# Kernel tuning notes

Hardware: AMD Instinct MI355X
Metric: run time of the kernel (lower is better)

Reference implementation:

```python
import jax, jax.numpy as jnp
import numpy as np

N_TOTAL = 100000   # total nodes across types
NP_TYPE = 50000    # nodes per type
NP_G = 50000       # nodes per metapath graph
E_G = 500000       # edges per metapath graph
NH = 4             # attention heads
HD = 64            # per-head hidden dim
HID = 64           # shared hidden dim (== in_dim)
D = NH * HD        # 256, semantic attention dim
OUT = 64
T = 20000          # target nodes per metapath


def setup_inputs() -> dict:
    key = jax.random.key(0)
    ks = jax.random.split(key, 20)
    inp = {
        "features0": jax.random.normal(ks[0], (NP_TYPE, 256), jnp.float32),
        "features1": jax.random.normal(ks[1], (NP_TYPE, 256), jnp.float32),
        "fc_W": jax.random.normal(ks[2], (2, HID, 256), jnp.float32) * 0.06,
        "fc_b": jnp.zeros((2, HID), jnp.float32),
        "gat_W": jax.random.normal(ks[3], (2, 2, HID, D), jnp.float32) * 0.12,
        "attn_l": jax.random.normal(ks[4], (2, 2, NH, HD), jnp.float32) * 0.12,
        "attn_r": jax.random.normal(ks[5], (2, 2, NH, HD), jnp.float32) * 0.12,
        "sem_W": jax.random.normal(ks[6], (2, D, D), jnp.float32) * 0.06,
        "sem_b": jnp.zeros((2, D), jnp.float32),
        "sem_q": jax.random.normal(ks[7], (2, D), jnp.float32) * 0.06,
        "fcout_W": jax.random.normal(ks[8], (2, D, OUT), jnp.float32) * 0.06,
        "fcout_b": jnp.zeros((2, OUT), jnp.float32),
        # static index structure (== np.where(type_mask == i))
        "type_idx": jnp.arange(2 * NP_TYPE, dtype=jnp.int32).reshape(2, NP_TYPE),
        "node_idx": jax.random.randint(ks[9], (2, 2, NP_G), 0, N_TOTAL, jnp.int32),
        "edge_src": jax.random.randint(ks[10], (2, 2, E_G), 0, NP_G, jnp.int32),
        "edge_dst": jax.random.randint(ks[11], (2, 2, E_G), 0, NP_G, jnp.int32),
        "tgt_idx": jax.random.randint(ks[12], (2, 2, T), 0, NP_G, jnp.int32),
    }
    return inp


def _gat(h, W, al, ar, src, dst):
    # h: [NP_G, HID] -> multi-head GAT -> [NP_G, NH*HD]
    z = (h @ W).reshape(NP_G, NH, HD)
    el = jnp.sum(z * al, axis=-1)                     # [NP_G, NH]
    er = jnp.sum(z * ar, axis=-1)
    e = jax.nn.leaky_relu(el[src] + er[dst], 0.2)     # [E, NH]
    emax = jax.ops.segment_max(e, dst, num_segments=NP_G)
    emax = jnp.where(jnp.isfinite(emax), emax, 0.0)
    ex = jnp.exp(e - emax[dst])
    denom = jax.ops.segment_sum(ex, dst, num_segments=NP_G)
    alpha = ex / (denom[dst] + 1e-9)                  # edge softmax over in-edges
    out = jax.ops.segment_sum(alpha[:, :, None] * z[src], dst, num_segments=NP_G)
    return jax.nn.elu(out).reshape(NP_G, D)


def _semantic(zs, Wm, bm, qm):
    # zs: [T, M, D] metapath-specific embeddings
    w = jnp.mean(jnp.tanh(zs @ Wm + bm) @ qm, axis=0)  # [M]
    beta = jax.nn.softmax(w)
    return jnp.einsum('tmd,m->td', zs, beta)


def reference(features0, features1, fc_W, fc_b, gat_W, attn_l, attn_r,
              sem_W, sem_b, sem_q, fcout_W, fcout_b,
              type_idx, node_idx, edge_src, edge_dst, tgt_idx):
    # type-based linear + scatter into shared node-feature tensor
    transformed = jnp.zeros((N_TOTAL, HID), dtype=features0.dtype)
    transformed = transformed.at[type_idx[0]].set(features0 @ fc_W[0].T + fc_b[0])
    transformed = transformed.at[type_idx[1]].set(features1 @ fc_W[1].T + fc_b[1])

    outs = []
    for b in range(2):          # two HAN branches (gene, dis)
        metas = []
        for m in range(2):      # metapaths per branch
            h = transformed[node_idx[b, m]]            # gather metapath node feats
            o = _gat(h, gat_W[b, m], attn_l[b, m], attn_r[b, m],
                     edge_src[b, m], edge_dst[b, m])
            metas.append(o[tgt_idx[b, m]])             # select target nodes
        zs = jnp.stack(metas, axis=1)                  # [T, M, D]
        s = _semantic(zs, sem_W[b], sem_b[b], sem_q[b])
        outs.append(s @ fcout_W[b] + fcout_b[b])
    return jnp.stack(outs)  # [2, T, OUT]
```

## Files before the change

kernel.cpp:

```cpp
#include <hip/hip_runtime.h>
#include <math.h>

#define NT     100000
#define NPT    50000
#define NPG    50000
#define EG     500000
#define DD     256
#define TT     20000
#define NPB    196
#define AGGB   2048

typedef __attribute__((ext_vector_type(8))) short short8;
typedef __attribute__((ext_vector_type(4))) float f32x4;
typedef unsigned short u16;

#define MFMA16(a, b, c) __builtin_amdgcn_mfma_f32_16x16x32_bf16((a), (b), (c), 0, 0, 0)

__device__ inline unsigned pk2(float x, float y) {
    unsigned a = __float_as_uint(x); a = (a + 0x7FFFu + ((a >> 16) & 1u)) >> 16;
    unsigned b = __float_as_uint(y); b = (b + 0x7FFFu + ((b >> 16) & 1u)) >> 16;
    return (a & 0xFFFFu) | (b << 16);
}
__device__ inline u16 pkb(float x) {
    unsigned a = __float_as_uint(x);
    return (u16)((a + 0x7FFFu + ((a >> 16) & 1u)) >> 16);
}
__device__ inline short8 cvt8(float4 a, float4 b) {
    union { int4 i; short8 s; } u;
    u.i = make_int4((int)pk2(a.x, a.y), (int)pk2(a.z, a.w),
                    (int)pk2(b.x, b.y), (int)pk2(b.z, b.w));
    return u.s;
}
__device__ inline float4 up4(unsigned lo, unsigned hi) {
    float4 r;
    r.x = __uint_as_float(lo << 16);
    r.y = __uint_as_float(lo & 0xFFFF0000u);
    r.z = __uint_as_float(hi << 16);
    r.w = __uint_as_float(hi & 0xFFFF0000u);
    return r;
}
__device__ inline float uplo(unsigned w) { return __uint_as_float(w << 16); }
__device__ inline float uphi(unsigned w) { return __uint_as_float(w & 0xFFFF0000u); }
__device__ inline float ftanh(float x) {
    float e = __expf(2.f * x);
    return 1.f - 2.f * __builtin_amdgcn_rcpf(e + 1.f);
}

__global__ __launch_bounds__(256) void prep_kernel(
    const float* __restrict__ fcW, const float* __restrict__ gatW,
    const float* __restrict__ semW, const float* __restrict__ foW,
    u16* __restrict__ fcWb, u16* __restrict__ gatWb,
    u16* __restrict__ semWb, u16* __restrict__ foWb)
{
    int i = blockIdx.x * 256 + threadIdx.x;
    if (i < 32768) fcWb[i] = pkb(fcW[i]);
    if (i < 65536) {
        int g = i >> 14, rem = i & 16383, n = rem >> 6, k = rem & 63;
        gatWb[i] = pkb(gatW[g * 16384 + k * 256 + n]);
    }
    if (i < 131072) {
        int b = i >> 16, rem = i & 65535, n = rem >> 8, k = rem & 255;
        semWb[i] = pkb(semW[b * 65536 + k * 256 + n]);
    }
    if (i < 32768) {
        int b = i >> 14, rem = i & 16383, n = rem >> 8, k = rem & 255;
        foWb[i] = pkb(foW[b * 16384 + k * 64 + n]);
    }
}

__global__ __launch_bounds__(256) void fc_kernel(
    const float* __restrict__ f0, const float* __restrict__ f1,
    const u16* __restrict__ fcWb, const float* __restrict__ fcb,
    const int* __restrict__ type_idx, u16* __restrict__ tbf)
{
    __shared__ short As[64 * 256];
    __shared__ short Bs[64 * 256];
    int ty = blockIdx.y;
    const float* feat = ty ? f1 : f0;
    const u16* W = fcWb + ty * 64 * 256;
    int tid = threadIdx.x, wv = tid >> 6, l = tid & 63, q = l >> 4, c = l & 15;
    int rbase = blockIdx.x * 64;
    short8 bv[8];
#pragma unroll
    for (int j = 0; j < 8; ++j)
        bv[j] = *(const short8*)&W[(tid + 256 * j) * 8];
    const float* Abase = feat + (size_t)rbase * 256;
#pragma unroll
    for (int half = 0; half < 2; ++half) {
        float4 va[8];
#pragma unroll
        for (int j = 0; j < 8; ++j) {
            int fi = tid + 256 * (half * 8 + j);
            bool okA = (rbase + (fi >> 6)) < NPT;
            va[j] = okA ? *(const float4*)(Abase + (size_t)fi * 4)
                        : (float4){0.f, 0.f, 0.f, 0.f};
        }
#pragma unroll
        for (int j = 0; j < 8; ++j) {
            int fi = tid + 256 * (half * 8 + j);
            int r = fi >> 6, cs = (fi & 63) * 4;
            int2 v = make_int2((int)pk2(va[j].x, va[j].y),
                               (int)pk2(va[j].z, va[j].w));
            *(int2*)&As[r * 256 + (cs ^ ((r & 15) << 3))] = v;
        }
    }
#pragma unroll
    for (int j = 0; j < 8; ++j) {
        int e = tid + 256 * j, r = e >> 5, cs = (e & 31) * 8;
        *(short8*)&Bs[r * 256 + (cs ^ ((r & 15) << 3))] = bv[j];
    }
    __syncthreads();
    short8 af[8];
    int arow = wv * 16 + c;
#pragma unroll
    for (int s = 0; s < 8; ++s)
        af[s] = *(const short8*)&As[arow * 256 + ((q * 8 + 32 * s) ^ (c << 3))];
    f32x4 acc[4];
#pragma unroll
    for (int i = 0; i < 4; ++i) acc[i] = (f32x4){0.f, 0.f, 0.f, 0.f};
#pragma unroll
    for (int s = 0; s < 8; ++s)
#pragma unroll
        for (int t4 = 0; t4 < 4; ++t4)
            acc[t4] = MFMA16(af[s],
                *(const short8*)&Bs[(t4 * 16 + c) * 256 +
                                    ((q * 8 + 32 * s) ^ (c << 3))], acc[t4]);
    int grl = rbase + wv * 16 + q * 4;
#pragma unroll
    for (int t4 = 0; t4 < 4; ++t4) {
        int col = t4 * 16 + c;
        float bvv = fcb[ty * 64 + col];
#pragma unroll
        for (int reg = 0; reg < 4; ++reg) {
            int gr = grl + reg;
            if (gr < NPT) {
                int dest = type_idx[ty * NPT + gr];
                tbf[(size_t)dest * 64 + col] = pkb(acc[t4][reg] + bvv);
            }
        }
    }
}

__global__ __launch_bounds__(256) void z_kernel(
    const u16* __restrict__ tbf, const int* __restrict__ nidx4,
    const u16* __restrict__ gatWb4, const float* __restrict__ al4,
    const float* __restrict__ ar4, u16* __restrict__ zb4,
    float* __restrict__ el4, float* __restrict__ er4, int g0)
{
    __shared__ short Bs[256 * 72];
    int gy = blockIdx.y, g = g0 + gy;
    const int* nidx = nidx4 + (size_t)g * NPG;
    const u16* gatWb = gatWb4 + (size_t)g * 16384;
    const float* al = al4 + g * 256;
    const float* ar = ar4 + g * 256;
    u16* zb = zb4 + (size_t)gy * NPG * 256;
    float* el = el4 + (size_t)gy * NPG * 4;
    float* er = er4 + (size_t)gy * NPG * 4;
    int tid = threadIdx.x, wv = tid >> 6, l = tid & 63, q = l >> 4, c = l & 15;
    short8 bv[8];
#pragma unroll
    for (int j = 0; j < 8; ++j)
        bv[j] = *(const short8*)&gatWb[(tid + 256 * j) * 8];
    int rbase = blockIdx.x * 64;
    int row = rbase + wv * 16 + c;
    bool ok = row < NPG;
    short8 af0 = (short8)(short)0, af1 = (short8)(short)0;
    if (ok) {
        int n = nidx[row];
        const u16* Ap = tbf + (size_t)n * 64 + q * 8;
        af0 = *(const short8*)(Ap);
        af1 = *(const short8*)(Ap + 32);
    }
#pragma unroll
    for (int j = 0; j < 8; ++j) {
        int e = tid + 256 * j, r = e >> 3, kc = (e & 7) * 8;
        *(short8*)&Bs[r * 72 + kc] = bv[j];
    }
    __syncthreads();
    f32x4 acc[16];
    const f32x4 zero = (f32x4){0.f, 0.f, 0.f, 0.f};
#pragma unroll
    for (int t16 = 0; t16 < 16; ++t16) {
        const short* Bp = &Bs[(t16 * 16 + c) * 72 + q * 8];
        acc[t16] = MFMA16(af0, *(const short8*)&Bp[0], zero);
        acc[t16] = MFMA16(af1, *(const short8*)&Bp[32], acc[t16]);
    }
    int grl = rbase + wv * 16 + q * 4;
#pragma unroll
    for (int t16 = 0; t16 < 16; ++t16)
#pragma unroll
        for (int reg = 0; reg < 4; ++reg) {
            int gr = grl + reg;
            if (gr < NPG)
                zb[(size_t)gr * 256 + t16 * 16 + c] = pkb(acc[t16][reg]);
        }
    float pl[4][4], pr[4][4];
#pragma unroll
    for (int reg = 0; reg < 4; ++reg)
#pragma unroll
        for (int h = 0; h < 4; ++h) { pl[reg][h] = 0.f; pr[reg][h] = 0.f; }
#pragma unroll
    for (int t16 = 0; t16 < 16; ++t16) {
        int col = t16 * 16 + c, h = t16 >> 2;
        float alv = al[col], arv = ar[col];
#pragma unroll
        for (int reg = 0; reg < 4; ++reg) {
            pl[reg][h] += acc[t16][reg] * alv;
            pr[reg][h] += acc[t16][reg] * arv;
        }
    }
#pragma unroll
    for (int o = 1; o < 16; o <<= 1)
#pragma unroll
        for (int reg = 0; reg < 4; ++reg)
#pragma unroll
            for (int h = 0; h < 4; ++h) {
                pl[reg][h] += __shfl_xor(pl[reg][h], o);
                pr[reg][h] += __shfl_xor(pr[reg][h], o);
            }
    if (c == 0) {
#pragma unroll
        for (int reg = 0; reg < 4; ++reg) {
            int gr = grl + reg;
            if (gr < NPG) {
                float4 vl = {pl[reg][0], pl[reg][1], pl[reg][2], pl[reg][3]};
                float4 vr = {pr[reg][0], pr[reg][1], pr[reg][2], pr[reg][3]};
                *(float4*)&el[gr * 4] = vl;
                *(float4*)&er[gr * 4] = vr;
            }
        }
    }
}

__global__ __launch_bounds__(256) void mark_kernel(
    const int* __restrict__ tgt, int* __restrict__ tflag4)
{
    int g = blockIdx.y;
    int i = blockIdx.x * 256 + threadIdx.x;
    if (i < TT) tflag4[g * NPG + tgt[(size_t)g * TT + i]] = 1;
}

__global__ __launch_bounds__(256) void count4_kernel(
    const int* __restrict__ dst, const int* __restrict__ tflag4,
    int* __restrict__ deg4)
{
    int g = blockIdx.y;
    int e = blockIdx.x * 256 + threadIdx.x;
    if (e < EG) {
        int d = dst[(size_t)g * EG + e];
        if (tflag4[g * NPG + d]) atomicAdd(&deg4[g * NPG + d], 1);
    }
}

__device__ inline int block_excl_scan(int v, int tid) {
    __shared__ int wtot[4];
    int lane = tid & 63, w = tid >> 6;
    int x = v;
#pragma unroll
    for (int o = 1; o < 64; o <<= 1) {
        int y = __shfl_up(x, o);
        if (lane >= o) x += y;
    }
    if (lane == 63) wtot[w] = x;
    __syncthreads();
    if (tid == 0) {
        int s = 0;
#pragma unroll
        for (int i = 0; i < 4; ++i) { int t = wtot[i]; wtot[i] = s; s += t; }
    }
    __syncthreads();
    return wtot[w] + x - v;
}

__global__ __launch_bounds__(256) void partial4_kernel(
    const int* __restrict__ deg4, int* __restrict__ part4)
{
    int g = blockIdx.y;
    int i = blockIdx.x * 256 + threadIdx.x;
    int v = (i < NPG) ? deg4[g * NPG + i] : 0;
#pragma unroll
    for (int o = 32; o > 0; o >>= 1) v += __shfl_xor(v, o);
    __shared__ int ws4[4];
    if ((threadIdx.x & 63) == 0) ws4[threadIdx.x >> 6] = v;
    __syncthreads();
    if (threadIdx.x == 0)
        part4[g * NPB + blockIdx.x] = ws4[0] + ws4[1] + ws4[2] + ws4[3];
}

__global__ __launch_bounds__(256) void scanp_kernel(
    const int* __restrict__ part4, int* __restrict__ pref4,
    int* __restrict__ offsets4)
{
    int g = blockIdx.y;
    int t = threadIdx.x;
    int v = (t < NPB) ? part4[g * NPB + t] : 0;
    int e = block_excl_scan(v, t);
    if (t < NPB) pref4[g * NPB + t] = e;
    if (t == 255) offsets4[(size_t)g * (NPG + 1) + NPG] = e + v;
}

__global__ __launch_bounds__(256) void distribute_kernel(
    const int* __restrict__ deg4, const int* __restrict__ pref4,
    int* __restrict__ offsets4, int* __restrict__ cursor4)
{
    int g = blockIdx.y;
    int i = blockIdx.x * 256 + threadIdx.x;
    int v = (i < NPG) ? deg4[g * NPG + i] : 0;
    int e = block_excl_scan(v, threadIdx.x);
    if (i < NPG) {
        int off = pref4[g * NPB + blockIdx.x] + e;
        offsets4[(size_t)g * (NPG + 1) + i] = off;
        cursor4[g * NPG + i] = off;
    }
}

__global__ __launch_bounds__(256) void scatter4_kernel(
    const int* __restrict__ dst, const int* __restrict__ src,
    const int* __restrict__ tflag4, int* __restrict__ cursor4,
    int* __restrict__ perm4, int* __restrict__ dpm4)
{
    int g = blockIdx.y;
    int e = blockIdx.x * 256 + threadIdx.x;
    if (e < EG) {
        int d = dst[(size_t)g * EG + e];
        if (tflag4[g * NPG + d]) {
            int pos = atomicAdd(&cursor4[g * NPG + d], 1);
            perm4[(size_t)g * EG + pos] = src[(size_t)g * EG + e];
            dpm4[(size_t)g * EG + pos] = d;
        }
    }
}

__global__ __launch_bounds__(256) void tpack_kernel(
    const int* __restrict__ tgt4, const int* __restrict__ offsets4,
    int2* __restrict__ tp4)
{
    int g = blockIdx.y;
    int i = blockIdx.x * 256 + threadIdx.x;
    if (i < TT) {
        int d = tgt4[(size_t)g * TT + i];
        const int* o = offsets4 + (size_t)g * (NPG + 1) + d;
        tp4[(size_t)g * TT + i] = make_int2(o[0], o[1]);
    }
}

__global__ __launch_bounds__(256) void escore_kernel(
    const int* __restrict__ perm4, const int* __restrict__ dpm4,
    const int* __restrict__ offsets4, const float* __restrict__ el4,
    const float* __restrict__ er4, float* __restrict__ elp4, int g0)
{
    int gy = blockIdx.y, g = g0 + gy;
    int i = blockIdx.x * 256 + threadIdx.x;
    int total = offsets4[(size_t)g * (NPG + 1) + NPG];
    if (i < total) {
        int s = perm4[(size_t)g * EG + i];
        int d = dpm4[(size_t)g * EG + i];
        float4 a = *(const float4*)&el4[(size_t)gy * NPG * 4 + s * 4];
        float4 b = *(const float4*)&er4[(size_t)gy * NPG * 4 + d * 4];
        float4 v;
        v.x = a.x + b.x; v.x = fmaxf(v.x, 0.2f * v.x);
        v.y = a.y + b.y; v.y = fmaxf(v.y, 0.2f * v.y);
        v.z = a.z + b.z; v.z = fmaxf(v.z, 0.2f * v.z);
        v.w = a.w + b.w; v.w = fmaxf(v.w, 0.2f * v.w);
        *(float4*)&elp4[(size_t)gy * EG * 4 + (size_t)i * 4] = v;
    }
}

__global__ __launch_bounds__(256) void agg_kernel(
    const int* __restrict__ tgt4, const int2* __restrict__ tp4,
    const int* __restrict__ perm4, const float* __restrict__ elp4,
    const float* __restrict__ el4, const float* __restrict__ er4,
    const u16* __restrict__ zb4, u16* __restrict__ metab4, int g0)
{
    int gy = blockIdx.y, g = g0 + gy;
    const int2* tp = tp4 + (size_t)g * TT;
    const int* perm = perm4 + (size_t)g * EG;
    const float* elp = elp4 ? elp4 + (size_t)gy * EG * 4 : (const float*)0;
    const u16* zb = zb4 + (size_t)gy * NPG * 256;
    u16* metab = metab4 + (size_t)g * TT * 256;
    int lane = threadIdx.x & 63;
    int h1 = lane & 3, e0l = lane >> 2, h2 = lane >> 4;
    const u16* zrow = zb + (size_t)lane * 4;
    const int nwaves = AGGB * 4;
    int wid0 = blockIdx.x * 4 + (threadIdx.x >> 6);

    for (int t = wid0; t < TT; t += nwaves) {
        int2 se = tp[t];
        int start = se.x, deg = se.y - se.x;
        int pv = perm[start + (lane < deg ? lane : 0)];
        float mx = -INFINITY;
        float a0 = 0.f, a1 = 0.f, a2 = 0.f, a3 = 0.f, dn = 0.f;
        if (elp) {
            const float* es = elp + (size_t)start * 4;
            for (int ee = e0l; ee < deg; ee += 16)
                mx = fmaxf(mx, es[ee * 4 + h1]);
#pragma unroll
            for (int o = 4; o < 64; o <<= 1) mx = fmaxf(mx, __shfl_xor(mx, o));
            float mxh = __shfl(mx, h2);
            int it = 0, dega = deg & ~3;
            for (; it < dega; it += 4) {
                int s0 = (it + 0 < 64) ? __shfl(pv, it + 0) : perm[start + it + 0];
                int s1 = (it + 1 < 64) ? __shfl(pv, it + 1) : perm[start + it + 1];
                int s2 = (it + 2 < 64) ? __shfl(pv, it + 2) : perm[start + it + 2];
                int s3 = (it + 3 < 64) ? __shfl(pv, it + 3) : perm[start + it + 3];
                float c0 = es[(it + 0) * 4 + h2];
                float c1 = es[(it + 1) * 4 + h2];
                float c2 = es[(it + 2) * 4 + h2];
                float c3 = es[(it + 3) * 4 + h2];
                uint2 w0 = *(const uint2*)&zrow[(size_t)s0 * 256];
                uint2 w1 = *(const uint2*)&zrow[(size_t)s1 * 256];
                uint2 w2 = *(const uint2*)&zrow[(size_t)s2 * 256];
                uint2 w3 = *(const uint2*)&zrow[(size_t)s3 * 256];
                float x0 = __expf(c0 - mxh), x1 = __expf(c1 - mxh);
                float x2 = __expf(c2 - mxh), x3 = __expf(c3 - mxh);
                dn += (x0 + x1) + (x2 + x3);
                a0 += x0 * uplo(w0.x) + x1 * uplo(w1.x)
                    + x2 * uplo(w2.x) + x3 * uplo(w3.x);
                a1 += x0 * uphi(w0.x) + x1 * uphi(w1.x)
                    + x2 * uphi(w2.x) + x3 * uphi(w3.x);
                a2 += x0 * uplo(w0.y) + x1 * uplo(w1.y)
                    + x2 * uplo(w2.y) + x3 * uplo(w3.y);
                a3 += x0 * uphi(w0.y) + x1 * uphi(w1.y)
                    + x2 * uphi(w2.y) + x3 * uphi(w3.y);
            }
            for (; it < deg; ++it) {
                int s = (it < 64) ? __shfl(pv, it) : perm[start + it];
                float c = es[it * 4 + h2];
                uint2 w = *(const uint2*)&zrow[(size_t)s * 256];
                float x = __expf(c - mxh);
                dn += x;
                a0 += x * uplo(w.x); a1 += x * uphi(w.x);
                a2 += x * uplo(w.y); a3 += x * uphi(w.y);
            }
        } else {
            const float* el = el4 + (size_t)gy * NPG * 4;
            const float* er = er4 + (size_t)gy * NPG * 4;
            int dstn = tgt4[(size_t)g * TT + t];
            float erv1 = er[dstn * 4 + h1];
            for (int ee = e0l; ee < deg; ee += 16) {
                int s = (ee < 64) ? __shfl(pv, ee) : perm[start + ee];
                float v = el[s * 4 + h1] + erv1; v = fmaxf(v, 0.2f * v);
                mx = fmaxf(mx, v);
            }
#pragma unroll
            for (int o = 4; o < 64; o <<= 1) mx = fmaxf(mx, __shfl_xor(mx, o));
            float mxh = __shfl(mx, h2);
            float erv2 = er[dstn * 4 + h2];
            for (int it = 0; it < deg; ++it) {
                int s = (it < 64) ? __shfl(pv, it) : perm[start + it];
                float v = el[s * 4 + h2] + erv2; v = fmaxf(v, 0.2f * v);
                float x = __expf(v - mxh);
                dn += x;
                uint2 w = *(const uint2*)&zrow[(size_t)s * 256];
                a0 += x * uplo(w.x); a1 += x * uphi(w.x);
                a2 += x * uplo(w.y); a3 += x * uphi(w.y);
            }
        }
        float inv = __builtin_amdgcn_rcpf(dn + 1e-9f);
        float v0 = a0 * inv, v1 = a1 * inv, v2 = a2 * inv, v3 = a3 * inv;
        v0 = v0 > 0.f ? v0 : (__expf(v0) - 1.f);
        v1 = v1 > 0.f ? v1 : (__expf(v1) - 1.f);
        v2 = v2 > 0.f ? v2 : (__expf(v2) - 1.f);
        v3 = v3 > 0.f ? v3 : (__expf(v3) - 1.f);
        uint2 mw;
        mw.x = pk2(v0, v1); mw.y = pk2(v2, v3);
        *(uint2*)&metab[(size_t)t * 256 + lane * 4] = mw;
    }
}

__global__ __launch_bounds__(256) void sem_kernel(
    const u16* __restrict__ metab4, const u16* __restrict__ semWb,
    const float* __restrict__ semb, const float* __restrict__ semq,
    float* __restrict__ wsum4)
{
    __shared__ short Bs[64 * 264];
    __shared__ float bsum;
    int g = blockIdx.y, b = g >> 1;
    const u16* A = metab4 + (size_t)g * TT * 256;
    int tid = threadIdx.x, wv = tid >> 6, l = tid & 63, q = l >> 4, c = l & 15;
    if (tid == 0) bsum = 0.f;
    int rbase = blockIdx.x * 64;
    int row = rbase + wv * 16 + c;
    bool ok = row < TT;
    short8 af[8];
    const u16* Ap = A + (size_t)row * 256 + q * 8;
#pragma unroll
    for (int s = 0; s < 8; ++s)
        af[s] = ok ? *(const short8*)(Ap + 32 * s) : (short8)(short)0;
    float part = 0.f;
    int grl = rbase + wv * 16 + q * 4;
    for (int nq = 0; nq < 4; ++nq) {
        const u16* W = semWb + b * 65536 + nq * 16384;
        short8 bv[8];
#pragma unroll
        for (int j = 0; j < 8; ++j)
            bv[j] = *(const short8*)&W[(tid + 256 * j) * 8];
        __syncthreads();
#pragma unroll
        for (int j = 0; j < 8; ++j) {
            int e = tid + 256 * j, r = e >> 5, kc = (e & 31) * 8;
            *(short8*)&Bs[r * 264 + kc] = bv[j];
        }
        __syncthreads();
        f32x4 acc[4];
#pragma unroll
        for (int i = 0; i < 4; ++i) acc[i] = (f32x4){0.f, 0.f, 0.f, 0.f};
#pragma unroll
        for (int s = 0; s < 8; ++s)
#pragma unroll
            for (int t4 = 0; t4 < 4; ++t4)
                acc[t4] = MFMA16(af[s],
                    *(const short8*)&Bs[(t4 * 16 + c) * 264 + q * 8 + 32 * s], acc[t4]);
#pragma unroll
        for (int t4 = 0; t4 < 4; ++t4) {
            int col = nq * 64 + t4 * 16 + c;
            float bb = semb[b * 256 + col], qq = semq[b * 256 + col];
#pragma unroll
            for (int reg = 0; reg < 4; ++reg)
                if (grl + reg < TT) part += ftanh(acc[t4][reg] + bb) * qq;
        }
    }
    for (int o = 32; o > 0; o >>= 1) part += __shfl_xor(part, o);
    if (l == 0) atomicAdd(&bsum, part);
    __syncthreads();
    if (tid == 0) atomicAdd(&wsum4[g], bsum);
}

__global__ __launch_bounds__(256) void out_kernel(
    const u16* __restrict__ metab4, const float* __restrict__ wsum4,
    const u16* __restrict__ foWb, const float* __restrict__ fob,
    float* __restrict__ out)
{
    __shared__ short Bs[64 * 264];
    int b = blockIdx.y;
    int tid = threadIdx.x, wv = tid >> 6, l = tid & 63, q = l >> 4, c = l & 15;
    float w0 = wsum4[b * 2] * (1.f / TT), w1 = wsum4[b * 2 + 1] * (1.f / TT);
    float mxv = fmaxf(w0, w1);
    float e0 = __expf(w0 - mxv), e1 = __expf(w1 - mxv);
    float inv = 1.f / (e0 + e1);
    float b0 = e0 * inv, b1 = e1 * inv;
    const u16* W = foWb + b * 16384;
    short8 bv[8];
#pragma unroll
    for (int j = 0; j < 8; ++j)
        bv[j] = *(const short8*)&W[(tid + 256 * j) * 8];
    int rbase = blockIdx.x * 64;
    int row = rbase + wv * 16 + c;
    bool ok = row < TT;
    const u16* Ap0 = metab4 + (size_t)(b * 2) * TT * 256 + (size_t)row * 256 + q * 8;
    const u16* Ap1 = Ap0 + (size_t)TT * 256;
    short8 af[8];
#pragma unroll
    for (int half = 0; half < 2; ++half) {
        union { short8 s8; uint4 u; } ua[4], uc[4];
#pragma unroll
        for (int s = 0; s < 4; ++s) {
            int ss = half * 4 + s;
            ua[s].s8 = ok ? *(const short8*)(Ap0 + 32 * ss) : (short8)(short)0;
            uc[s].s8 = ok ? *(const short8*)(Ap1 + 32 * ss) : (short8)(short)0;
        }
        if (half == 0) {
#pragma unroll
            for (int j = 0; j < 8; ++j) {
                int e = tid + 256 * j, r = e >> 5, kc = (e & 31) * 8;
                *(short8*)&Bs[r * 264 + kc] = bv[j];
            }
        }
#pragma unroll
        for (int s = 0; s < 4; ++s) {
            float4 a0 = up4(ua[s].u.x, ua[s].u.y), a1 = up4(ua[s].u.z, ua[s].u.w);
            float4 c0 = up4(uc[s].u.x, uc[s].u.y), c1 = up4(uc[s].u.z, uc[s].u.w);
            float4 v0, v1;
            v0.x = b0 * a0.x + b1 * c0.x; v0.y = b0 * a0.y + b1 * c0.y;
            v0.z = b0 * a0.z + b1 * c0.z; v0.w = b0 * a0.w + b1 * c0.w;
            v1.x = b0 * a1.x + b1 * c1.x; v1.y = b0 * a1.y + b1 * c1.y;
            v1.z = b0 * a1.z + b1 * c1.z; v1.w = b0 * a1.w + b1 * c1.w;
            af[half * 4 + s] = cvt8(v0, v1);
        }
    }
    __syncthreads();
    f32x4 acc[4];
#pragma unroll
    for (int i = 0; i < 4; ++i) acc[i] = (f32x4){0.f, 0.f, 0.f, 0.f};
#pragma unroll
    for (int s = 0; s < 8; ++s)
#pragma unroll
        for (int t4 = 0; t4 < 4; ++t4)
            acc[t4] = MFMA16(af[s],
                *(const short8*)&Bs[(t4 * 16 + c) * 264 + q * 8 + 32 * s], acc[t4]);
    int grl = rbase + wv * 16 + q * 4;
#pragma unroll
    for (int t4 = 0; t4 < 4; ++t4) {
        int col = t4 * 16 + c;
        float bvv = fob[b * 64 + col];
#pragma unroll
        for (int reg = 0; reg < 4; ++reg) {
            int gr = grl + reg;
            if (gr < TT)
                out[(size_t)b * TT * 64 + (size_t)gr * 64 + col] = acc[t4][reg] + bvv;
        }
    }
}

extern "C" void kernel_launch(void* const* d_in, const int* in_sizes, int n_in,
                              void* d_out, int out_size, void* d_ws, size_t ws_size,
                              hipStream_t stream)
{
    const float* f0    = (const float*)d_in[0];
    const float* f1    = (const float*)d_in[1];
    const float* fcW   = (const float*)d_in[2];
    const float* fcb   = (const float*)d_in[3];
    const float* gatW  = (const float*)d_in[4];
    const float* al    = (const float*)d_in[5];
    const float* ar    = (const float*)d_in[6];
    const float* semW  = (const float*)d_in[7];
    const float* semb  = (const float*)d_in[8];
    const float* semq  = (const float*)d_in[9];
    const float* foW   = (const float*)d_in[10];
    const float* fob   = (const float*)d_in[11];
    const int* type_idx = (const int*)d_in[12];
    const int* node_idx = (const int*)d_in[13];
    const int* edge_src = (const int*)d_in[14];
    const int* edge_dst = (const int*)d_in[15];
    const int* tgt_idx  = (const int*)d_in[16];
    float* out = (float*)d_out;

    char* ws = (char*)d_ws;
    size_t off = 0;
    auto alloc = [&](size_t bytes) -> void* {
        void* p = ws + off;
        off = (off + bytes + 255) & ~(size_t)255;
        return p;
    };
    u16*   tbf         = (u16*)alloc((size_t)NT * 64 * 2);
    u16*   metab4      = (u16*)alloc((size_t)4 * TT * 256 * 2);
    float* wsum4       = (float*)alloc(64);
    u16*   fcWb        = (u16*)alloc(32768 * 2);
    u16*   gatWb       = (u16*)alloc(65536 * 2);
    u16*   semWb       = (u16*)alloc(131072 * 2);
    u16*   foWb        = (u16*)alloc(32768 * 2);
    int*   deg4        = (int*)alloc((size_t)4 * NPG * 4);
    int*   tflag4      = (int*)alloc((size_t)4 * NPG * 4);
    int*   offsets4    = (int*)alloc((size_t)4 * (NPG + 1) * 4);
    int*   cursor4     = (int*)alloc((size_t)4 * NPG * 4);
    int*   perm4       = (int*)alloc((size_t)4 * EG * 4);
    int*   dpm4        = (int*)alloc((size_t)4 * EG * 4);
    int2*  tp4         = (int2*)alloc((size_t)4 * TT * 8);
    int*   part4       = (int*)alloc((size_t)4 * NPB * 4);
    int*   pref4       = (int*)alloc((size_t)4 * NPB * 4);
    const size_t perg_base = (size_t)NPG * 256 * 2 + 2 * (size_t)NPG * 4 * 4 + 768;
    const size_t perg_elp  = perg_base + (size_t)EG * 16 + 256;
    int GPB = 1; bool use_elp = false;
    {
        size_t rem = (ws_size > off) ? ws_size - off : 0;
        if      (rem >= 4 * perg_elp)  { GPB = 4; use_elp = true;  }
        else if (rem >= 4 * perg_base) { GPB = 4; use_elp = false; }
        else if (rem >= 2 * perg_elp)  { GPB = 2; use_elp = true;  }
        else if (rem >= 2 * perg_base) { GPB = 2; use_elp = false; }
        else if (rem >= 1 * perg_elp)  { GPB = 1; use_elp = true;  }
    }
    u16*   zb          = (u16*)alloc((size_t)GPB * NPG * 256 * 2);
    float* el          = (float*)alloc((size_t)GPB * NPG * 4 * 4);
    float* er          = (float*)alloc((size_t)GPB * NPG * 4 * 4);
    float* elp         = use_elp ? (float*)alloc((size_t)GPB * EG * 16) : (float*)0;

    const int eblocks = (EG + 255) / 256;
    const int tblocks = (TT + 255) / 256;

    prep_kernel<<<512, 256, 0, stream>>>(fcW, gatW, semW, foW,
                                         fcWb, gatWb, semWb, foWb);

    hipMemsetAsync(deg4, 0, (size_t)4 * NPG * 4, stream);
    hipMemsetAsync(tflag4, 0, (size_t)4 * NPG * 4, stream);
    hipMemsetAsync(wsum4, 0, 16, stream);
    mark_kernel<<<dim3(tblocks, 4), 256, 0, stream>>>(tgt_idx, tflag4);
    count4_kernel<<<dim3(eblocks, 4), 256, 0, stream>>>(edge_dst, tflag4, deg4);
    partial4_kernel<<<dim3(NPB, 4), 256, 0, stream>>>(deg4, part4);
    scanp_kernel<<<dim3(1, 4), 256, 0, stream>>>(part4, pref4, offsets4);
    distribute_kernel<<<dim3(NPB, 4), 256, 0, stream>>>(deg4, pref4, offsets4,
                                                        cursor4);
    tpack_kernel<<<dim3(tblocks, 4), 256, 0, stream>>>(tgt_idx, offsets4, tp4);
    scatter4_kernel<<<dim3(eblocks, 4), 256, 0, stream>>>(edge_dst, edge_src,
                                                          tflag4, cursor4,
                                                          perm4, dpm4);

    fc_kernel<<<dim3(782, 2), 256, 0, stream>>>(f0, f1, fcWb, fcb, type_idx, tbf);
    for (int g0 = 0; g0 < 4; g0 += GPB) {
        z_kernel<<<dim3(782, GPB), 256, 0, stream>>>(
            tbf, node_idx, gatWb, al, ar, zb, el, er, g0);
        if (elp)
            escore_kernel<<<dim3(eblocks, GPB), 256, 0, stream>>>(
                perm4, dpm4, offsets4, el, er, elp, g0);
        agg_kernel<<<dim3(AGGB, GPB), 256, 0, stream>>>(
            tgt_idx, tp4, perm4, elp, el, er, zb, metab4, g0);
    }
    sem_kernel<<<dim3(313, 4), 256, 0, stream>>>(metab4, semWb, semb, semq,
                                                 wsum4);
    out_kernel<<<dim3(313, 2), 256, 0, stream>>>(metab4, wsum4, foWb, fob, out);
}
```

Measured before the change: 454.2 us.

## Persist z_kernel tiles and widen agg gathers to 16-byte half-wave loads

z_kernel becomes persistent: each block loads the GAT weight tile into shared memory once and loops over several 64-row tiles, so the weight staging is no longer repeated for every tile. agg_kernel now has each half-wave read a full 512-byte z row with uint4 loads, handling two edges per step and combining the halves with a cross-half shuffle. AGGB drops from 2048 to 512. This targets weight reloads and narrow gather transactions, at the cost of fewer blocks in flight and more registers per lane.

```diff
diff --git a/kernel.cpp b/kernel.cpp
--- a/kernel.cpp
+++ b/kernel.cpp
@@ -8,7 +8,9 @@
 #define DD     256
 #define TT     20000
 #define NPB    196
-#define AGGB   2048
+#define AGGB   512
+#define ZTB    256
+#define NTILE  782
 
 typedef __attribute__((ext_vector_type(8))) short short8;
 typedef __attribute__((ext_vector_type(4))) float f32x4;
@@ -157,76 +159,81 @@
     float* el = el4 + (size_t)gy * NPG * 4;
     float* er = er4 + (size_t)gy * NPG * 4;
     int tid = threadIdx.x, wv = tid >> 6, l = tid & 63, q = l >> 4, c = l & 15;
-    short8 bv[8];
-#pragma unroll
-    for (int j = 0; j < 8; ++j)
-        bv[j] = *(const short8*)&gatWb[(tid + 256 * j) * 8];
-    int rbase = blockIdx.x * 64;
-    int row = rbase + wv * 16 + c;
-    bool ok = row < NPG;
-    short8 af0 = (short8)(short)0, af1 = (short8)(short)0;
-    if (ok) {
-        int n = nidx[row];
-        const u16* Ap = tbf + (size_t)n * 64 + q * 8;
-        af0 = *(const short8*)(Ap);
-        af1 = *(const short8*)(Ap + 32);
-    }
-#pragma unroll
-    for (int j = 0; j < 8; ++j) {
-        int e = tid + 256 * j, r = e >> 3, kc = (e & 7) * 8;
-        *(short8*)&Bs[r * 72 + kc] = bv[j];
+    {
+        short8 bv[8];
+#pragma unroll
+        for (int j = 0; j < 8; ++j)
+            bv[j] = *(const short8*)&gatWb[(tid + 256 * j) * 8];
+#pragma unroll
+        for (int j = 0; j < 8; ++j) {
+            int e = tid + 256 * j, r = e >> 3, kc = (e & 7) * 8;
+            *(short8*)&Bs[r * 72 + kc] = bv[j];
+        }
     }
     __syncthreads();
-    f32x4 acc[16];
-    const f32x4 zero = (f32x4){0.f, 0.f, 0.f, 0.f};
-#pragma unroll
-    for (int t16 = 0; t16 < 16; ++t16) {
-        const short* Bp = &Bs[(t16 * 16 + c) * 72 + q * 8];
-        acc[t16] = MFMA16(af0, *(const short8*)&Bp[0], zero);
-        acc[t16] = MFMA16(af1, *(const short8*)&Bp[32], acc[t16]);
-    }
-    int grl = rbase + wv * 16 + q * 4;
-#pragma unroll
-    for (int t16 = 0; t16 < 16; ++t16)
-#pragma unroll
-        for (int reg = 0; reg < 4; ++reg) {
-            int gr = grl + reg;
-            if (gr < NPG)
-                zb[(size_t)gr * 256 + t16 * 16 + c] = pkb(acc[t16][reg]);
-        }
-    float pl[4][4], pr[4][4];
-#pragma unroll
-    for (int reg = 0; reg < 4; ++reg)
-#pragma unroll
-        for (int h = 0; h < 4; ++h) { pl[reg][h] = 0.f; pr[reg][h] = 0.f; }
-#pragma unroll
-    for (int t16 = 0; t16 < 16; ++t16) {
-        int col = t16 * 16 + c, h = t16 >> 2;
-        float alv = al[col], arv = ar[col];
-#pragma unroll
-        for (int reg = 0; reg < 4; ++reg) {
-            pl[reg][h] += acc[t16][reg] * alv;
-            pr[reg][h] += acc[t16][reg] * arv;
-        }
-    }
-#pragma unroll
-    for (int o = 1; o < 16; o <<= 1)
+
+    for (int tile = blockIdx.x; tile < NTILE; tile += ZTB) {
+        int rbase = tile * 64;
+        int row = rbase + wv * 16 + c;
+        bool ok = row < NPG;
+        short8 af0 = (short8)(short)0, af1 = (short8)(short)0;
+        if (ok) {
+            int n = nidx[row];
+            const u16* Ap = tbf + (size_t)n * 64 + q * 8;
+            af0 = *(const short8*)(Ap);
+            af1 = *(const short8*)(Ap + 32);
+        }
+        f32x4 acc[16];
+        const f32x4 zero = (f32x4){0.f, 0.f, 0.f, 0.f};
+#pragma unroll
+        for (int t16 = 0; t16 < 16; ++t16) {
+            const short* Bp = &Bs[(t16 * 16 + c) * 72 + q * 8];
+            acc[t16] = MFMA16(af0, *(const short8*)&Bp[0], zero);
+            acc[t16] = MFMA16(af1, *(const short8*)&Bp[32], acc[t16]);
+        }
+        int grl = rbase + wv * 16 + q * 4;
+#pragma unroll
+        for (int t16 = 0; t16 < 16; ++t16)
+#pragma unroll
+            for (int reg = 0; reg < 4; ++reg) {
+                int gr = grl + reg;
+                if (gr < NPG)
+                    zb[(size_t)gr * 256 + t16 * 16 + c] = pkb(acc[t16][reg]);
+            }
+        float pl[4][4], pr[4][4];
 #pragma unroll
         for (int reg = 0; reg < 4; ++reg)
 #pragma unroll
-            for (int h = 0; h < 4; ++h) {
-                pl[reg][h] += __shfl_xor(pl[reg][h], o);
-                pr[reg][h] += __shfl_xor(pr[reg][h], o);
-            }
-    if (c == 0) {
-#pragma unroll
-        for (int reg = 0; reg < 4; ++reg) {
-            int gr = grl + reg;
-            if (gr < NPG) {
-                float4 vl = {pl[reg][0], pl[reg][1], pl[reg][2], pl[reg][3]};
-                float4 vr = {pr[reg][0], pr[reg][1], pr[reg][2], pr[reg][3]};
-                *(float4*)&el[gr * 4] = vl;
-                *(float4*)&er[gr * 4] = vr;
+            for (int h = 0; h < 4; ++h) { pl[reg][h] = 0.f; pr[reg][h] = 0.f; }
+#pragma unroll
+        for (int t16 = 0; t16 < 16; ++t16) {
+            int col = t16 * 16 + c, h = t16 >> 2;
+            float alv = al[col], arv = ar[col];
+#pragma unroll
+            for (int reg = 0; reg < 4; ++reg) {
+                pl[reg][h] += acc[t16][reg] * alv;
+                pr[reg][h] += acc[t16][reg] * arv;
+            }
+        }
+#pragma unroll
+        for (int o = 1; o < 16; o <<= 1)
+#pragma unroll
+            for (int reg = 0; reg < 4; ++reg)
+#pragma unroll
+                for (int h = 0; h < 4; ++h) {
+                    pl[reg][h] += __shfl_xor(pl[reg][h], o);
+                    pr[reg][h] += __shfl_xor(pr[reg][h], o);
+                }
+        if (c == 0) {
+#pragma unroll
+            for (int reg = 0; reg < 4; ++reg) {
+                int gr = grl + reg;
+                if (gr < NPG) {
+                    float4 vl = {pl[reg][0], pl[reg][1], pl[reg][2], pl[reg][3]};
+                    float4 vr = {pr[reg][0], pr[reg][1], pr[reg][2], pr[reg][3]};
+                    *(float4*)&el[gr * 4] = vl;
+                    *(float4*)&er[gr * 4] = vr;
+                }
             }
         }
     }
@@ -376,61 +383,66 @@
     const int2* tp = tp4 + (size_t)g * TT;
     const int* perm = perm4 + (size_t)g * EG;
     const float* elp = elp4 ? elp4 + (size_t)gy * EG * 4 : (const float*)0;
-    const u16* zb = zb4 + (size_t)gy * NPG * 256;
+    const char* zbb = (const char*)(zb4 + (size_t)gy * NPG * 256);
     u16* metab = metab4 + (size_t)g * TT * 256;
     int lane = threadIdx.x & 63;
-    int h1 = lane & 3, e0l = lane >> 2, h2 = lane >> 4;
-    const u16* zrow = zb + (size_t)lane * 4;
+    int half = lane >> 5, sl = lane & 31;
+    int h = sl >> 3;
+    int h1 = lane & 3, e0l = lane >> 2;
+    unsigned dimoff = (unsigned)sl * 16;
     const int nwaves = AGGB * 4;
     int wid0 = blockIdx.x * 4 + (threadIdx.x >> 6);
 
     for (int t = wid0; t < TT; t += nwaves) {
         int2 se = tp[t];
         int start = se.x, deg = se.y - se.x;
-        int pv = perm[start + (lane < deg ? lane : 0)];
-        float mx = -INFINITY;
-        float a0 = 0.f, a1 = 0.f, a2 = 0.f, a3 = 0.f, dn = 0.f;
+        int pidx = start + (lane < deg ? lane : 0);
+        if (pidx >= EG) pidx = EG - 1;
+        int pv = perm[pidx];
+        float mx = -INFINITY, mxh;
+        float a0 = 0.f, a1 = 0.f, a2 = 0.f, a3 = 0.f;
+        float a4 = 0.f, a5 = 0.f, a6 = 0.f, a7 = 0.f, dn = 0.f;
+
         if (elp) {
             const float* es = elp + (size_t)start * 4;
             for (int ee = e0l; ee < deg; ee += 16)
                 mx = fmaxf(mx, es[ee * 4 + h1]);
 #pragma unroll
             for (int o = 4; o < 64; o <<= 1) mx = fmaxf(mx, __shfl_xor(mx, o));
-            float mxh = __shfl(mx, h2);
-            int it = 0, dega = deg & ~3;
-            for (; it < dega; it += 4) {
-                int s0 = (it + 0 < 64) ? __shfl(pv, it + 0) : perm[start + it + 0];
-                int s1 = (it + 1 < 64) ? __shfl(pv, it + 1) : perm[start + it + 1];
-                int s2 = (it + 2 < 64) ? __shfl(pv, it + 2) : perm[start + it + 2];
-                int s3 = (it + 3 < 64) ? __shfl(pv, it + 3) : perm[start + it + 3];
-                float c0 = es[(it + 0) * 4 + h2];
-                float c1 = es[(it + 1) * 4 + h2];
-                float c2 = es[(it + 2) * 4 + h2];
-                float c3 = es[(it + 3) * 4 + h2];
-                uint2 w0 = *(const uint2*)&zrow[(size_t)s0 * 256];
-                uint2 w1 = *(const uint2*)&zrow[(size_t)s1 * 256];
-                uint2 w2 = *(const uint2*)&zrow[(size_t)s2 * 256];
-                uint2 w3 = *(const uint2*)&zrow[(size_t)s3 * 256];
-                float x0 = __expf(c0 - mxh), x1 = __expf(c1 - mxh);
-                float x2 = __expf(c2 - mxh), x3 = __expf(c3 - mxh);
-                dn += (x0 + x1) + (x2 + x3);
-                a0 += x0 * uplo(w0.x) + x1 * uplo(w1.x)
-                    + x2 * uplo(w2.x) + x3 * uplo(w3.x);
-                a1 += x0 * uphi(w0.x) + x1 * uphi(w1.x)
-                    + x2 * uphi(w2.x) + x3 * uphi(w3.x);
-                a2 += x0 * uplo(w0.y) + x1 * uplo(w1.y)
-                    + x2 * uplo(w2.y) + x3 * uplo(w3.y);
-                a3 += x0 * uphi(w0.y) + x1 * uphi(w1.y)
-                    + x2 * uphi(w2.y) + x3 * uphi(w3.y);
-            }
-            for (; it < deg; ++it) {
-                int s = (it < 64) ? __shfl(pv, it) : perm[start + it];
-                float c = es[it * 4 + h2];
-                uint2 w = *(const uint2*)&zrow[(size_t)s * 256];
-                float x = __expf(c - mxh);
+            mxh = __shfl(mx, h);
+            int it = 0;
+            for (; it + 4 <= deg; it += 4) {
+                int eA = it + half, eB = it + 2 + half;
+                int sA = (eA < 64) ? __shfl(pv, eA) : perm[start + eA];
+                int sB = (eB < 64) ? __shfl(pv, eB) : perm[start + eB];
+                float cA = es[eA * 4 + h];
+                float cB = es[eB * 4 + h];
+                uint4 wA = *(const uint4*)(zbb + (((unsigned)sA << 9) | dimoff));
+                uint4 wB = *(const uint4*)(zbb + (((unsigned)sB << 9) | dimoff));
+                float xA = __expf(cA - mxh), xB = __expf(cB - mxh);
+                dn += xA + xB;
+                a0 += xA * uplo(wA.x) + xB * uplo(wB.x);
+                a1 += xA * uphi(wA.x) + xB * uphi(wB.x);
+                a2 += xA * uplo(wA.y) + xB * uplo(wB.y);
+                a3 += xA * uphi(wA.y) + xB * uphi(wB.y);
+                a4 += xA * uplo(wA.z) + xB * uplo(wB.z);
+                a5 += xA * uphi(wA.z) + xB * uphi(wB.z);
+                a6 += xA * uplo(wA.w) + xB * uplo(wB.w);
+                a7 += xA * uphi(wA.w) + xB * uphi(wB.w);
+            }
+            for (; it < deg; it += 2) {
+                int e = it + half;
+                bool val = e < deg;
+                int ee = val ? e : it;
+                int s = (ee < 64) ? __shfl(pv, ee) : perm[start + ee];
+                float c = es[ee * 4 + h];
+                uint4 w = *(const uint4*)(zbb + (((unsigned)s << 9) | dimoff));
+                float x = val ? __expf(c - mxh) : 0.f;
                 dn += x;
                 a0 += x * uplo(w.x); a1 += x * uphi(w.x);
                 a2 += x * uplo(w.y); a3 += x * uphi(w.y);
+                a4 += x * uplo(w.z); a5 += x * uphi(w.z);
+                a6 += x * uplo(w.w); a7 += x * uphi(w.w);
             }
         } else {
             const float* el = el4 + (size_t)gy * NPG * 4;
@@ -444,27 +456,45 @@
             }
 #pragma unroll
             for (int o = 4; o < 64; o <<= 1) mx = fmaxf(mx, __shfl_xor(mx, o));
-            float mxh = __shfl(mx, h2);
-            float erv2 = er[dstn * 4 + h2];
-            for (int it = 0; it < deg; ++it) {
-                int s = (it < 64) ? __shfl(pv, it) : perm[start + it];
-                float v = el[s * 4 + h2] + erv2; v = fmaxf(v, 0.2f * v);
-                float x = __expf(v - mxh);
+            mxh = __shfl(mx, h);
+            float ervh = er[dstn * 4 + h];
+            for (int it = 0; it < deg; it += 2) {
+                int e = it + half;
+                bool val = e < deg;
+                int ee = val ? e : it;
+                int s = (ee < 64) ? __shfl(pv, ee) : perm[start + ee];
+                float v = el[s * 4 + h] + ervh; v = fmaxf(v, 0.2f * v);
+                uint4 w = *(const uint4*)(zbb + (((unsigned)s << 9) | dimoff));
+                float x = val ? __expf(v - mxh) : 0.f;
                 dn += x;
-                uint2 w = *(const uint2*)&zrow[(size_t)s * 256];
                 a0 += x * uplo(w.x); a1 += x * uphi(w.x);
                 a2 += x * uplo(w.y); a3 += x * uphi(w.y);
-            }
-        }
+                a4 += x * uplo(w.z); a5 += x * uphi(w.z);
+                a6 += x * uplo(w.w); a7 += x * uphi(w.w);
+            }
+        }
+        dn += __shfl_xor(dn, 32);
+        a0 += __shfl_xor(a0, 32); a1 += __shfl_xor(a1, 32);
+        a2 += __shfl_xor(a2, 32); a3 += __shfl_xor(a3, 32);
+        a4 += __shfl_xor(a4, 32); a5 += __shfl_xor(a5, 32);
+        a6 += __shfl_xor(a6, 32); a7 += __shfl_xor(a7, 32);
         float inv = __builtin_amdgcn_rcpf(dn + 1e-9f);
         float v0 = a0 * inv, v1 = a1 * inv, v2 = a2 * inv, v3 = a3 * inv;
+        float v4 = a4 * inv, v5 = a5 * inv, v6 = a6 * inv, v7 = a7 * inv;
         v0 = v0 > 0.f ? v0 : (__expf(v0) - 1.f);
         v1 = v1 > 0.f ? v1 : (__expf(v1) - 1.f);
         v2 = v2 > 0.f ? v2 : (__expf(v2) - 1.f);
         v3 = v3 > 0.f ? v3 : (__expf(v3) - 1.f);
-        uint2 mw;
-        mw.x = pk2(v0, v1); mw.y = pk2(v2, v3);
-        *(uint2*)&metab[(size_t)t * 256 + lane * 4] = mw;
+        v4 = v4 > 0.f ? v4 : (__expf(v4) - 1.f);
+        v5 = v5 > 0.f ? v5 : (__expf(v5) - 1.f);
+        v6 = v6 > 0.f ? v6 : (__expf(v6) - 1.f);
+        v7 = v7 > 0.f ? v7 : (__expf(v7) - 1.f);
+        if (half == 0) {
+            uint4 mw;
+            mw.x = pk2(v0, v1); mw.y = pk2(v2, v3);
+            mw.z = pk2(v4, v5); mw.w = pk2(v6, v7);
+            *(uint4*)&metab[(size_t)t * 256 + sl * 8] = mw;
+        }
     }
 }
 
@@ -686,7 +716,7 @@
 
     fc_kernel<<<dim3(782, 2), 256, 0, stream>>>(f0, f1, fcWb, fcb, type_idx, tbf);
     for (int g0 = 0; g0 < 4; g0 += GPB) {
-        z_kernel<<<dim3(782, GPB), 256, 0, stream>>>(
+        z_kernel<<<dim3(ZTB, GPB), 256, 0, stream>>>(
             tbf, node_idx, gatWb, al, ar, zb, el, er, g0);
         if (elp)
             escore_kernel<<<dim3(eblocks, GPB), 256, 0, stream>>>(
```

Measured after the change: 491.7 us. 1.08x slower.
